# Performance work log

Measured on AMD Instinct MI355X. Metric: run time of the kernel, lower is better.

The kernel has to match this reference:

```python
import jax, jax.numpy as jnp
import numpy as np

B, D, C = 16384, 1024, 2048


def setup_inputs() -> dict:
    key = jax.random.key(0)
    k1, k2 = jax.random.split(key)
    x = jax.random.normal(k1, (B, D), dtype=jnp.float32)
    # xavier_uniform for centers of shape (C, D): bound = sqrt(6/(C+D))
    bound = float(np.sqrt(6.0 / (C + D)))
    centers = jax.random.uniform(k2, (C, D), dtype=jnp.float32, minval=-bound, maxval=bound)
    gamma = jnp.ones((1,), dtype=jnp.float32)
    return {"x": x, "centers": centers, "gamma": gamma}


def _rbf(x, centers, gamma):
    # then Euclidean norm (sqrt) and exp(-gamma * dist) as in the torch module.
    x2 = jnp.sum(x * x, axis=-1, keepdims=True)            # (B, 1)
    c2 = jnp.sum(centers * centers, axis=-1)               # (C,)
    sq = x2 - 2.0 * jnp.einsum('bd,cd->bc', x, centers) + c2[None, :]
    dist = jnp.sqrt(jnp.maximum(sq, 0.0))                  # (B, C)
    return jnp.exp(-gamma[0] * dist)


def reference(x, centers, gamma):
    return _rbf(x, centers, gamma)
```

## Files before the change

kernel.cpp:

```cpp
#include <hip/hip_runtime.h>
#include <stdint.h>


typedef __attribute__((ext_vector_type(4))) int i32x4;

#define BM 128
#define BN 128
#define BK 128

__global__ __launch_bounds__(256) void prep_i8(
    const float* __restrict__ in, unsigned char* __restrict__ qb,
    float2* __restrict__ info, int K) {
  int row = blockIdx.x;
  int tid = threadIdx.x;
  float4 v = ((const float4*)(in + (size_t)row * K))[tid];
  float ss = v.x * v.x + v.y * v.y + v.z * v.z + v.w * v.w;
  float am = fmaxf(fmaxf(fabsf(v.x), fabsf(v.y)), fmaxf(fabsf(v.z), fabsf(v.w)));
  for (int off = 32; off > 0; off >>= 1) {
    ss += __shfl_down(ss, off, 64);
    am = fmaxf(am, __shfl_down(am, off, 64));
  }
  __shared__ float pss[4], pam[4], sbc;
  int lane = tid & 63, w = tid >> 6;
  if (lane == 0) { pss[w] = ss; pam[w] = am; }
  __syncthreads();
  if (tid == 0) {
    float tss = pss[0] + pss[1] + pss[2] + pss[3];
    float tam = fmaxf(fmaxf(pam[0], pam[1]), fmaxf(pam[2], pam[3]));
    float s = tam > 0.f ? 127.f / tam : 0.f;
    info[row] = make_float2(tss, tam * (1.f / 127.f));
    sbc = s;
  }
  __syncthreads();
  float s = sbc;
  int qx = __float2int_rn(v.x * s), qy = __float2int_rn(v.y * s);
  int qz = __float2int_rn(v.z * s), qw = __float2int_rn(v.w * s);
  unsigned u = (unsigned)(qx & 255) | ((unsigned)(qy & 255) << 8) |
               ((unsigned)(qz & 255) << 16) | ((unsigned)(qw & 255) << 24);
  ((unsigned*)qb)[(size_t)row * (K >> 2) + tid] = u;
}

#define GLDS(gptr, lptr)                                                      \
  __builtin_amdgcn_global_load_lds(                                           \
      (const __attribute__((address_space(1))) unsigned int*)(gptr),          \
      (__attribute__((address_space(3))) unsigned int*)(lptr), 16, 0, 0)

#define DSR(dst, addr, imm)                                                   \
  asm volatile("ds_read_b128 %0, %1 offset:%c2"                              \
               : "=v"(dst) : "v"(addr), "i"(imm))

#define BARRIER __builtin_amdgcn_s_barrier()
#define LGKM(n)                                                               \
  do {                                                                        \
    asm volatile("s_waitcnt lgkmcnt(" #n ")" ::: "memory");                   \
    __builtin_amdgcn_sched_barrier(0);                                        \
  } while (0)
#define VMW(n) asm volatile("s_waitcnt vmcnt(" #n ")" ::: "memory")

#define MFMAI8(a, b, c) __builtin_amdgcn_mfma_i32_16x16x64_i8((a), (b), (c), 0, 0, 0)

__global__ __launch_bounds__(256) void rbf_gemm_i8(
    const unsigned char* __restrict__ A, const unsigned char* __restrict__ Bm,
    const float2* __restrict__ xinfo, const float2* __restrict__ cinfo,
    const float* __restrict__ gamma, float* __restrict__ out,
    int M, int N, int K) {
  __shared__ __align__(16) unsigned char lds[2 * 32768];

  int nbn = N / BN;
  int nwg = (M / BM) * nbn;
  int bid = blockIdx.x;
  int wg = bid;
  if ((nwg & 7) == 0) {
    int cpx = nwg >> 3;
    wg = (bid & 7) * cpx + (bid >> 3);
  }
  int bm = wg / nbn, bn = wg % nbn;

  int tid = threadIdx.x;
  int lane = tid & 63, wv = tid >> 6;
  int wm = wv >> 1;
  int wn = wv & 1;
  int l15 = lane & 15, l4 = lane >> 4;

  const size_t Kz = (size_t)K;

  int lsw = (tid & 7) ^ ((tid >> 3) & 7);
  const unsigned char* AgT = A + (size_t)bm * BM * Kz + (size_t)(tid >> 3) * Kz + lsw * 16;
  const unsigned char* BgT = Bm + (size_t)bn * BN * Kz + (size_t)(tid >> 3) * Kz + lsw * 16;
  size_t r32 = (size_t)32 * Kz;

#define STG8(TAU, BUFS)                                                       \
  do {                                                                        \
    GLDS(AgT + (size_t)(TAU) * 128, (BUFS) + tid * 16);                       \
    GLDS(AgT + r32 + (size_t)(TAU) * 128, (BUFS) + 4096 + tid * 16);          \
    GLDS(AgT + 2 * r32 + (size_t)(TAU) * 128, (BUFS) + 8192 + tid * 16);      \
    GLDS(AgT + 3 * r32 + (size_t)(TAU) * 128, (BUFS) + 12288 + tid * 16);     \
    GLDS(BgT + (size_t)(TAU) * 128, (BUFS) + 16384 + tid * 16);               \
    GLDS(BgT + r32 + (size_t)(TAU) * 128, (BUFS) + 20480 + tid * 16);         \
    GLDS(BgT + 2 * r32 + (size_t)(TAU) * 128, (BUFS) + 24576 + tid * 16);     \
    GLDS(BgT + 3 * r32 + (size_t)(TAU) * 128, (BUFS) + 28672 + tid * 16);     \
  } while (0)

  int psl = l4 ^ (l15 & 7);
  unsigned ldsBase =
      (unsigned)(size_t)(const __attribute__((address_space(3))) void*)&lds[0];
  unsigned aBase = ldsBase + (unsigned)(wm * 8192 + l15 * 128 + psl * 16);
  unsigned bBase = ldsBase + (unsigned)(16384 + wn * 8192 + l15 * 128 + psl * 16);

  i32x4 acc[4][4];
#pragma unroll
  for (int m = 0; m < 4; ++m)
#pragma unroll
    for (int n = 0; n < 4; ++n) acc[m][n] = (i32x4){0, 0, 0, 0};

  int nt = K / BK;

  STG8(0, lds);
  VMW(0);
  BARRIER;

  for (int t = 0; t < nt; ++t) {
    unsigned bufOff = (unsigned)(t & 1) * 32768u;
    unsigned char* bufS = lds + ((t + 1) & 1) * 32768;

    unsigned aAd0 = aBase + bufOff;
    unsigned bAd0 = bBase + bufOff;
    unsigned aAd1 = aAd0 ^ 64u;
    unsigned bAd1 = bAd0 ^ 64u;

    i32x4 a0, a1, a2, a3, b0, b1, b2, b3;
    i32x4 a4, a5, a6, a7, b4, b5, b6, b7;
    DSR(a0, aAd0, 0);    DSR(a1, aAd0, 2048);
    DSR(a2, aAd0, 4096); DSR(a3, aAd0, 6144);
    DSR(b0, bAd0, 0);    DSR(b1, bAd0, 2048);
    DSR(b2, bAd0, 4096); DSR(b3, bAd0, 6144);
    DSR(a4, aAd1, 0);    DSR(a5, aAd1, 2048);
    DSR(a6, aAd1, 4096); DSR(a7, aAd1, 6144);
    DSR(b4, bAd1, 0);    DSR(b5, bAd1, 2048);
    DSR(b6, bAd1, 4096); DSR(b7, bAd1, 6144);
    if (t + 1 < nt) STG8(t + 1, bufS);

    LGKM(8);
    __builtin_amdgcn_s_setprio(1);
    acc[0][0] = MFMAI8(a0, b0, acc[0][0]);
    acc[0][1] = MFMAI8(a0, b1, acc[0][1]);
    acc[0][2] = MFMAI8(a0, b2, acc[0][2]);
    acc[0][3] = MFMAI8(a0, b3, acc[0][3]);
    acc[1][0] = MFMAI8(a1, b0, acc[1][0]);
    acc[1][1] = MFMAI8(a1, b1, acc[1][1]);
    acc[1][2] = MFMAI8(a1, b2, acc[1][2]);
    acc[1][3] = MFMAI8(a1, b3, acc[1][3]);
    acc[2][0] = MFMAI8(a2, b0, acc[2][0]);
    acc[2][1] = MFMAI8(a2, b1, acc[2][1]);
    acc[2][2] = MFMAI8(a2, b2, acc[2][2]);
    acc[2][3] = MFMAI8(a2, b3, acc[2][3]);
    acc[3][0] = MFMAI8(a3, b0, acc[3][0]);
    acc[3][1] = MFMAI8(a3, b1, acc[3][1]);
    acc[3][2] = MFMAI8(a3, b2, acc[3][2]);
    acc[3][3] = MFMAI8(a3, b3, acc[3][3]);
    LGKM(0);
    acc[0][0] = MFMAI8(a4, b4, acc[0][0]);
    acc[0][1] = MFMAI8(a4, b5, acc[0][1]);
    acc[0][2] = MFMAI8(a4, b6, acc[0][2]);
    acc[0][3] = MFMAI8(a4, b7, acc[0][3]);
    acc[1][0] = MFMAI8(a5, b4, acc[1][0]);
    acc[1][1] = MFMAI8(a5, b5, acc[1][1]);
    acc[1][2] = MFMAI8(a5, b6, acc[1][2]);
    acc[1][3] = MFMAI8(a5, b7, acc[1][3]);
    acc[2][0] = MFMAI8(a6, b4, acc[2][0]);
    acc[2][1] = MFMAI8(a6, b5, acc[2][1]);
    acc[2][2] = MFMAI8(a6, b6, acc[2][2]);
    acc[2][3] = MFMAI8(a6, b7, acc[2][3]);
    acc[3][0] = MFMAI8(a7, b4, acc[3][0]);
    acc[3][1] = MFMAI8(a7, b5, acc[3][1]);
    acc[3][2] = MFMAI8(a7, b6, acc[3][2]);
    acc[3][3] = MFMAI8(a7, b7, acc[3][3]);
    __builtin_amdgcn_s_setprio(0);

    if (t < nt - 1) {
      VMW(0);
      BARRIER;
    }
  }

  float g = gamma[0];
  int rb0 = bm * BM + wm * 64 + l4 * 4;
  int cb0 = bn * BN + wn * 64 + l15;
#pragma unroll
  for (int m = 0; m < 4; ++m) {
#pragma unroll
    for (int j = 0; j < 4; ++j) {
      int row = rb0 + m * 16 + j;
      float2 xi = xinfo[row];
      size_t ob = (size_t)row * N;
#pragma unroll
      for (int n = 0; n < 4; ++n) {
        int col = cb0 + n * 16;
        float2 ci = cinfo[col];
        float dot = (float)acc[m][n][j] * xi.y * ci.y;
        float sq = fmaxf(xi.x + ci.x - 2.f * dot, 0.f);
        out[ob + col] = __expf(-g * __builtin_sqrtf(sq));
      }
    }
  }
}

__global__ __launch_bounds__(256) void rbf_naive(
    const float* __restrict__ x, const float* __restrict__ cent,
    const float* __restrict__ gamma, float* __restrict__ out, int D, int N) {
  int row = blockIdx.x;
  int col = blockIdx.y * blockDim.x + threadIdx.x;
  extern __shared__ float xs[];
  for (int i = threadIdx.x; i < D; i += blockDim.x)
    xs[i] = x[(size_t)row * D + i];
  __syncthreads();
  if (col >= N) return;
  const float* cp = cent + (size_t)col * D;
  float s = 0.f;
  for (int d = 0; d < D; ++d) {
    float df = xs[d] - cp[d];
    s += df * df;
  }
  out[(size_t)row * N + col] = __expf(-gamma[0] * __builtin_sqrtf(fmaxf(s, 0.f)));
}

extern "C" void kernel_launch(void* const* d_in, const int* in_sizes, int n_in,
                              void* d_out, int out_size, void* d_ws, size_t ws_size,
                              hipStream_t stream) {
  const float* x = (const float*)d_in[0];
  const float* cent = (const float*)d_in[1];
  const float* gamma = (const float*)d_in[2];
  float* out = (float*)d_out;

  const int D = 1024;
  int Brows = in_sizes[0] / D;
  int C = in_sizes[1] / D;

  size_t qa = (size_t)Brows * D;
  size_t qc = (size_t)C * D;
  size_t need = qa + qc + (size_t)Brows * 8 + (size_t)C * 8;
  bool can = (ws_size >= need) && (D == 1024) && (Brows % BM == 0) &&
             (C % BN == 0);

  if (!can) {
    dim3 grid(Brows, (C + 255) / 256);
    hipLaunchKernelGGL(rbf_naive, grid, dim3(256), D * sizeof(float), stream,
                       x, cent, gamma, out, D, C);
    return;
  }

  unsigned char* xb = (unsigned char*)d_ws;
  unsigned char* cb = xb + qa;
  float2* xinfo = (float2*)(xb + qa + qc);
  float2* cinfo = xinfo + Brows;

  hipLaunchKernelGGL(prep_i8, dim3(Brows), dim3(256), 0, stream, x, xb, xinfo, D);
  hipLaunchKernelGGL(prep_i8, dim3(C), dim3(256), 0, stream, cent, cb, cinfo, D);

  int nwg = (Brows / BM) * (C / BN);
  hipLaunchKernelGGL(rbf_gemm_i8, dim3(nwg), dim3(256), 0, stream,
                     xb, cb, xinfo, cinfo, gamma, out, Brows, C, D);
}
```

Before: 86.87 us.

## Switch GEMM from int8 MFMA to FP8 scaled MFMA 16x16x128

Quantizes x and centers to FP8 e4m3 (scale to 448) instead of int8, and replaces the int8 16x16x64 MFMA with the gfx950 scaled f8f6f4 16x16x128 MFMA that has neutral block scales. The LDS read pattern is reworked to build 32-byte operands from two 16-byte reads with an adjusted swizzle, and the two-phase wait is collapsed into a single wait. The aim is to halve the number of MFMA issues per K tile. The trade-offs are coarser FP8 precision on the dot product and less overlap between LDS reads and MFMAs.

```diff
diff --git a/kernel.cpp b/kernel.cpp
--- a/kernel.cpp
+++ b/kernel.cpp
@@ -1,14 +1,17 @@
 #include <hip/hip_runtime.h>
+#include <hip/hip_fp8.h>
 #include <stdint.h>
 
 
 typedef __attribute__((ext_vector_type(4))) int i32x4;
+typedef __attribute__((ext_vector_type(8))) int i32x8;
+typedef __attribute__((ext_vector_type(4))) float f32x4;
 
 #define BM 128
 #define BN 128
 #define BK 128
 
-__global__ __launch_bounds__(256) void prep_i8(
+__global__ __launch_bounds__(256) void prep_fp8(
     const float* __restrict__ in, unsigned char* __restrict__ qb,
     float2* __restrict__ info, int K) {
   int row = blockIdx.x;
@@ -27,16 +30,15 @@
   if (tid == 0) {
     float tss = pss[0] + pss[1] + pss[2] + pss[3];
     float tam = fmaxf(fmaxf(pam[0], pam[1]), fmaxf(pam[2], pam[3]));
-    float s = tam > 0.f ? 127.f / tam : 0.f;
-    info[row] = make_float2(tss, tam * (1.f / 127.f));
+    float s = tam > 0.f ? 448.f / tam : 0.f;
+    info[row] = make_float2(tss, tam * (1.f / 448.f));
     sbc = s;
   }
   __syncthreads();
   float s = sbc;
-  int qx = __float2int_rn(v.x * s), qy = __float2int_rn(v.y * s);
-  int qz = __float2int_rn(v.z * s), qw = __float2int_rn(v.w * s);
-  unsigned u = (unsigned)(qx & 255) | ((unsigned)(qy & 255) << 8) |
-               ((unsigned)(qz & 255) << 16) | ((unsigned)(qw & 255) << 24);
+  __hip_fp8_e4m3 q0(v.x * s), q1(v.y * s), q2(v.z * s), q3(v.w * s);
+  unsigned u = (unsigned)q0.__x | ((unsigned)q1.__x << 8) |
+               ((unsigned)q2.__x << 16) | ((unsigned)q3.__x << 24);
   ((unsigned*)qb)[(size_t)row * (K >> 2) + tid] = u;
 }
 
@@ -57,9 +59,19 @@
   } while (0)
 #define VMW(n) asm volatile("s_waitcnt vmcnt(" #n ")" ::: "memory")
 
-#define MFMAI8(a, b, c) __builtin_amdgcn_mfma_i32_16x16x64_i8((a), (b), (c), 0, 0, 0)
-
-__global__ __launch_bounds__(256) void rbf_gemm_i8(
+#define MFMAF8(a, b, c)                                                       \
+  __builtin_amdgcn_mfma_scale_f32_16x16x128_f8f6f4(                           \
+      (a), (b), (c), 0, 0, 0, 0x7F7F7F7F, 0, 0x7F7F7F7F)
+
+#define RD32(dst8, adLo, adHi, imm)                                           \
+  do {                                                                        \
+    i32x4 lo_, hi_;                                                           \
+    DSR(lo_, adLo, imm);                                                      \
+    DSR(hi_, adHi, imm);                                                      \
+    dst8 = __builtin_shufflevector(lo_, hi_, 0, 1, 2, 3, 4, 5, 6, 7);         \
+  } while (0)
+
+__global__ __launch_bounds__(256) void rbf_gemm_f8(
     const unsigned char* __restrict__ A, const unsigned char* __restrict__ Bm,
     const float2* __restrict__ xinfo, const float2* __restrict__ cinfo,
     const float* __restrict__ gamma, float* __restrict__ out,
@@ -101,17 +113,17 @@
     GLDS(BgT + 3 * r32 + (size_t)(TAU) * 128, (BUFS) + 28672 + tid * 16);     \
   } while (0)
 
-  int psl = l4 ^ (l15 & 7);
+  int psl = (2 * l4) ^ (l15 & 7);
   unsigned ldsBase =
       (unsigned)(size_t)(const __attribute__((address_space(3))) void*)&lds[0];
-  unsigned aBase = ldsBase + (unsigned)(wm * 8192 + l15 * 128 + psl * 16);
-  unsigned bBase = ldsBase + (unsigned)(16384 + wn * 8192 + l15 * 128 + psl * 16);
-
-  i32x4 acc[4][4];
+  unsigned aLoB = ldsBase + (unsigned)(wm * 8192 + l15 * 128 + psl * 16);
+  unsigned bLoB = ldsBase + (unsigned)(16384 + wn * 8192 + l15 * 128 + psl * 16);
+
+  f32x4 acc[4][4];
 #pragma unroll
   for (int m = 0; m < 4; ++m)
 #pragma unroll
-    for (int n = 0; n < 4; ++n) acc[m][n] = (i32x4){0, 0, 0, 0};
+    for (int n = 0; n < 4; ++n) acc[m][n] = (f32x4){0.f, 0.f, 0.f, 0.f};
 
   int nt = K / BK;
 
@@ -123,58 +135,38 @@
     unsigned bufOff = (unsigned)(t & 1) * 32768u;
     unsigned char* bufS = lds + ((t + 1) & 1) * 32768;
 
-    unsigned aAd0 = aBase + bufOff;
-    unsigned bAd0 = bBase + bufOff;
-    unsigned aAd1 = aAd0 ^ 64u;
-    unsigned bAd1 = bAd0 ^ 64u;
-
-    i32x4 a0, a1, a2, a3, b0, b1, b2, b3;
-    i32x4 a4, a5, a6, a7, b4, b5, b6, b7;
-    DSR(a0, aAd0, 0);    DSR(a1, aAd0, 2048);
-    DSR(a2, aAd0, 4096); DSR(a3, aAd0, 6144);
-    DSR(b0, bAd0, 0);    DSR(b1, bAd0, 2048);
-    DSR(b2, bAd0, 4096); DSR(b3, bAd0, 6144);
-    DSR(a4, aAd1, 0);    DSR(a5, aAd1, 2048);
-    DSR(a6, aAd1, 4096); DSR(a7, aAd1, 6144);
-    DSR(b4, bAd1, 0);    DSR(b5, bAd1, 2048);
-    DSR(b6, bAd1, 4096); DSR(b7, bAd1, 6144);
+    unsigned aLo = aLoB + bufOff, aHi = aLo ^ 16u;
+    unsigned bLo = bLoB + bufOff, bHi = bLo ^ 16u;
+
+    i32x8 af0, af1, af2, af3, bf0, bf1, bf2, bf3;
+    RD32(af0, aLo, aHi, 0);
+    RD32(af1, aLo, aHi, 2048);
+    RD32(af2, aLo, aHi, 4096);
+    RD32(af3, aLo, aHi, 6144);
+    RD32(bf0, bLo, bHi, 0);
+    RD32(bf1, bLo, bHi, 2048);
+    RD32(bf2, bLo, bHi, 4096);
+    RD32(bf3, bLo, bHi, 6144);
     if (t + 1 < nt) STG8(t + 1, bufS);
 
-    LGKM(8);
+    LGKM(0);
     __builtin_amdgcn_s_setprio(1);
-    acc[0][0] = MFMAI8(a0, b0, acc[0][0]);
-    acc[0][1] = MFMAI8(a0, b1, acc[0][1]);
-    acc[0][2] = MFMAI8(a0, b2, acc[0][2]);
-    acc[0][3] = MFMAI8(a0, b3, acc[0][3]);
-    acc[1][0] = MFMAI8(a1, b0, acc[1][0]);
-    acc[1][1] = MFMAI8(a1, b1, acc[1][1]);
-    acc[1][2] = MFMAI8(a1, b2, acc[1][2]);
-    acc[1][3] = MFMAI8(a1, b3, acc[1][3]);
-    acc[2][0] = MFMAI8(a2, b0, acc[2][0]);
-    acc[2][1] = MFMAI8(a2, b1, acc[2][1]);
-    acc[2][2] = MFMAI8(a2, b2, acc[2][2]);
-    acc[2][3] = MFMAI8(a2, b3, acc[2][3]);
-    acc[3][0] = MFMAI8(a3, b0, acc[3][0]);
-    acc[3][1] = MFMAI8(a3, b1, acc[3][1]);
-    acc[3][2] = MFMAI8(a3, b2, acc[3][2]);
-    acc[3][3] = MFMAI8(a3, b3, acc[3][3]);
-    LGKM(0);
-    acc[0][0] = MFMAI8(a4, b4, acc[0][0]);
-    acc[0][1] = MFMAI8(a4, b5, acc[0][1]);
-    acc[0][2] = MFMAI8(a4, b6, acc[0][2]);
-    acc[0][3] = MFMAI8(a4, b7, acc[0][3]);
-    acc[1][0] = MFMAI8(a5, b4, acc[1][0]);
-    acc[1][1] = MFMAI8(a5, b5, acc[1][1]);
-    acc[1][2] = MFMAI8(a5, b6, acc[1][2]);
-    acc[1][3] = MFMAI8(a5, b7, acc[1][3]);
-    acc[2][0] = MFMAI8(a6, b4, acc[2][0]);
-    acc[2][1] = MFMAI8(a6, b5, acc[2][1]);
-    acc[2][2] = MFMAI8(a6, b6, acc[2][2]);
-    acc[2][3] = MFMAI8(a6, b7, acc[2][3]);
-    acc[3][0] = MFMAI8(a7, b4, acc[3][0]);
-    acc[3][1] = MFMAI8(a7, b5, acc[3][1]);
-    acc[3][2] = MFMAI8(a7, b6, acc[3][2]);
-    acc[3][3] = MFMAI8(a7, b7, acc[3][3]);
+    acc[0][0] = MFMAF8(af0, bf0, acc[0][0]);
+    acc[0][1] = MFMAF8(af0, bf1, acc[0][1]);
+    acc[0][2] = MFMAF8(af0, bf2, acc[0][2]);
+    acc[0][3] = MFMAF8(af0, bf3, acc[0][3]);
+    acc[1][0] = MFMAF8(af1, bf0, acc[1][0]);
+    acc[1][1] = MFMAF8(af1, bf1, acc[1][1]);
+    acc[1][2] = MFMAF8(af1, bf2, acc[1][2]);
+    acc[1][3] = MFMAF8(af1, bf3, acc[1][3]);
+    acc[2][0] = MFMAF8(af2, bf0, acc[2][0]);
+    acc[2][1] = MFMAF8(af2, bf1, acc[2][1]);
+    acc[2][2] = MFMAF8(af2, bf2, acc[2][2]);
+    acc[2][3] = MFMAF8(af2, bf3, acc[2][3]);
+    acc[3][0] = MFMAF8(af3, bf0, acc[3][0]);
+    acc[3][1] = MFMAF8(af3, bf1, acc[3][1]);
+    acc[3][2] = MFMAF8(af3, bf2, acc[3][2]);
+    acc[3][3] = MFMAF8(af3, bf3, acc[3][3]);
     __builtin_amdgcn_s_setprio(0);
 
     if (t < nt - 1) {
@@ -197,7 +189,7 @@
       for (int n = 0; n < 4; ++n) {
         int col = cb0 + n * 16;
         float2 ci = cinfo[col];
-        float dot = (float)acc[m][n][j] * xi.y * ci.y;
+        float dot = acc[m][n][j] * xi.y * ci.y;
         float sq = fmaxf(xi.x + ci.x - 2.f * dot, 0.f);
         out[ob + col] = __expf(-g * __builtin_sqrtf(sq));
       }
@@ -254,10 +246,10 @@
   float2* xinfo = (float2*)(xb + qa + qc);
   float2* cinfo = xinfo + Brows;
 
-  hipLaunchKernelGGL(prep_i8, dim3(Brows), dim3(256), 0, stream, x, xb, xinfo, D);
-  hipLaunchKernelGGL(prep_i8, dim3(C), dim3(256), 0, stream, cent, cb, cinfo, D);
+  hipLaunchKernelGGL(prep_fp8, dim3(Brows), dim3(256), 0, stream, x, xb, xinfo, D);
+  hipLaunchKernelGGL(prep_fp8, dim3(C), dim3(256), 0, stream, cent, cb, cinfo, D);
 
   int nwg = (Brows / BM) * (C / BN);
-  hipLaunchKernelGGL(rbf_gemm_i8, dim3(nwg), dim3(256), 0, stream,
+  hipLaunchKernelGGL(rbf_gemm_f8, dim3(nwg), dim3(256), 0, stream,
                      xb, cb, xinfo, cinfo, gamma, out, Brows, C, D);
 }
```

Result: slower. 93.01 us (+7.1%).
